# Kernel tuning notes

Measured on AMD Instinct MI355X. Metric: run time of the kernel, lower is better.

## Reference

```python
import jax, jax.numpy as jnp
import numpy as np

N = 50000      # nodes
E = 800000     # edges (before self-loops)
DIN = 128      # input feature dim
DOUT = 128     # per-head output dim
H = 4          # heads (concat=False -> mean over heads)
SLOPE = 0.2    # PyG GATConv default negative_slope


def setup_inputs() -> dict:
    key = jax.random.key(0)
    k1, k2, k3, k4, k5 = jax.random.split(key, 5)
    x = jax.random.normal(k1, (N, DIN), dtype=jnp.float32)
    edge_index = jax.random.randint(k2, (2, E), 0, N)
    W = jax.random.normal(k3, (DIN, H * DOUT), dtype=jnp.float32) / np.sqrt(DIN).astype(np.float32)
    att_src = jax.random.normal(k4, (H, DOUT), dtype=jnp.float32) * 0.1
    att_dst = jax.random.normal(k5, (H, DOUT), dtype=jnp.float32) * 0.1
    return {"x": x, "edge_index": edge_index, "W": W, "att_src": att_src, "att_dst": att_dst}


def _gat(x, W, att_src, att_dst, src, dst):
    h = (x @ W).reshape(N, H, DOUT)                      # [N,H,C] shared lin for src/dst
    a_s = jnp.einsum('nhc,hc->nh', h, att_src)           # [N,H]
    a_d = jnp.einsum('nhc,hc->nh', h, att_dst)           # [N,H]
    logits = jax.nn.leaky_relu(a_s[src] + a_d[dst], SLOPE)   # [Etot,H]
    m = jax.ops.segment_max(logits, dst, num_segments=N)     # segment softmax (stable)
    e = jnp.exp(logits - m[dst])
    denom = jax.ops.segment_sum(e, dst, num_segments=N)
    alpha = e / (denom[dst] + 1e-16)                         # [Etot,H]
    out = jax.ops.segment_sum(alpha[:, :, None] * h[src], dst, num_segments=N)  # [N,H,C]
    return out.mean(axis=1)                                   # concat=False -> average heads


def reference(x, edge_index, W, att_src, att_dst):
    loop = jnp.arange(N, dtype=edge_index.dtype)          # add_self_loops=True (PyG default)
    src = jnp.concatenate([edge_index[0], loop])
    dst = jnp.concatenate([edge_index[1], loop])
    return _gat(x, W, att_src, att_dst, src, dst)
```

## Files before the change

### kernel.cpp

```cpp
#include <hip/hip_runtime.h>

#define NN 50000
#define EE 800000
#define ETOT (EE + NN)
#define MAXD 192
#define NBK 49
#define CAP 20480
#define CH 4096

typedef _Float16 f16x8 __attribute__((ext_vector_type(8)));
typedef _Float16 f16x2 __attribute__((ext_vector_type(2)));
typedef float f32x4 __attribute__((ext_vector_type(4)));
typedef unsigned int u32x4 __attribute__((ext_vector_type(4)));

__device__ __forceinline__ float lrelu(float v) { return v > 0.f ? v : 0.2f * v; }
__device__ __forceinline__ unsigned int pack2(float a, float b) {
  unsigned short lo = __builtin_bit_cast(unsigned short, (_Float16)a);
  unsigned short hi = __builtin_bit_cast(unsigned short, (_Float16)b);
  return (unsigned int)lo | ((unsigned int)hi << 16);
}

__global__ void k_prep(const float* __restrict__ W,
                       const float* __restrict__ att_s,
                       const float* __restrict__ att_d,
                       unsigned short* __restrict__ Bt,
                       float* __restrict__ WaS, float* __restrict__ WaD,
                       int* __restrict__ bcnt) {
  int gid = blockIdx.x * blockDim.x + threadIdx.x;
  if (gid < NBK) bcnt[gid] = 0;
  if (gid < 128 * 512) {
    int col = gid >> 9, k = gid & 511;
    float v = W[(k & 127) * 512 + (k >> 7) * 128 + col];
    _Float16 hv = (_Float16)v;
    Bt[col * 512 + k] = __builtin_bit_cast(unsigned short, hv);
  }
  if (gid < 512) {
    int k = gid >> 2, h = gid & 3;
    const float* wrow = W + k * 512 + h * 128;
    const float* as = att_s + h * 128;
    const float* ad = att_d + h * 128;
    float ss = 0.f, sd = 0.f;
    for (int c = 0; c < 128; ++c) { float w = wrow[c]; ss += w * as[c]; sd += w * ad[c]; }
    WaS[k * 4 + h] = ss;
    WaD[k * 4 + h] = sd;
  }
}

__global__ __launch_bounds__(256) void k_xcast(const float* __restrict__ x,
                                               const float* __restrict__ WaS,
                                               const float* __restrict__ WaD,
                                               unsigned int* __restrict__ xh,
                                               float* __restrict__ a_s,
                                               float* __restrict__ a_d) {
  __shared__ unsigned long long D[128][33];
  __shared__ float4 wsl[128];
  __shared__ float4 wdl[128];
  int t = threadIdx.x;
  int nb = blockIdx.x * 128;
  if (t < 128) wsl[t] = ((const float4*)WaS)[t];
  else wdl[t - 128] = ((const float4*)WaD)[t - 128];

#pragma unroll
  for (int i = 0; i < 16; ++i) {
    int idx = t + i * 256;
    int n = idx >> 5, c4 = idx & 31;
    int gn = nb + n;
    float4 v = make_float4(0.f, 0.f, 0.f, 0.f);
    if (gn < NN) v = ((const float4*)x)[(size_t)gn * 32 + c4];
    unsigned int lo = pack2(v.x, v.y);
    unsigned int hi = pack2(v.z, v.w);
    if (gn < NN) ((uint2*)xh)[(size_t)gn * 32 + c4] = make_uint2(lo, hi);
    D[n][c4] = (unsigned long long)lo | ((unsigned long long)hi << 32);
  }
  __syncthreads();

  int n = t >> 1, half = t & 1;
  float s0 = 0.f, s1 = 0.f, s2 = 0.f, s3 = 0.f;
  float d0 = 0.f, d1 = 0.f, d2 = 0.f, d3 = 0.f;
#pragma unroll
  for (int p = 0; p < 16; ++p) {
    int c4 = 2 * p + half;
    unsigned long long q = D[n][c4];
    f16x2 lo2 = __builtin_bit_cast(f16x2, (unsigned int)q);
    f16x2 hi2 = __builtin_bit_cast(f16x2, (unsigned int)(q >> 32));
    float f0 = (float)lo2[0], f1 = (float)lo2[1];
    float f2 = (float)hi2[0], f3 = (float)hi2[1];
    int c = c4 * 4;
    float4 w0 = wsl[c], w1 = wsl[c + 1], w2 = wsl[c + 2], w3 = wsl[c + 3];
    s0 += f0 * w0.x + f1 * w1.x + f2 * w2.x + f3 * w3.x;
    s1 += f0 * w0.y + f1 * w1.y + f2 * w2.y + f3 * w3.y;
    s2 += f0 * w0.z + f1 * w1.z + f2 * w2.z + f3 * w3.z;
    s3 += f0 * w0.w + f1 * w1.w + f2 * w2.w + f3 * w3.w;
    float4 v0 = wdl[c], v1 = wdl[c + 1], v2 = wdl[c + 2], v3 = wdl[c + 3];
    d0 += f0 * v0.x + f1 * v1.x + f2 * v2.x + f3 * v3.x;
    d1 += f0 * v0.y + f1 * v1.y + f2 * v2.y + f3 * v3.y;
    d2 += f0 * v0.z + f1 * v1.z + f2 * v2.z + f3 * v3.z;
    d3 += f0 * v0.w + f1 * v1.w + f2 * v2.w + f3 * v3.w;
  }
  s0 += __shfl_xor(s0, 1); s1 += __shfl_xor(s1, 1);
  s2 += __shfl_xor(s2, 1); s3 += __shfl_xor(s3, 1);
  d0 += __shfl_xor(d0, 1); d1 += __shfl_xor(d1, 1);
  d2 += __shfl_xor(d2, 1); d3 += __shfl_xor(d3, 1);
  int gn = nb + n;
  if (half == 0 && gn < NN) {
    *(float4*)(a_s + gn * 4) = make_float4(s0, s1, s2, s3);
    *(float4*)(a_d + gn * 4) = make_float4(d0, d1, d2, d3);
  }
}

__global__ __launch_bounds__(256) void k_p1(const int* __restrict__ ei,
                                            int* __restrict__ bcnt,
                                            unsigned int* __restrict__ ebuf) {
  __shared__ int cnt[NBK];
  __shared__ int gbase[NBK];
  int t = threadIdx.x;
  int e0 = blockIdx.x * CH;
  for (int i = t; i < NBK; i += 256) cnt[i] = 0;
  __syncthreads();
#pragma unroll
  for (int i = 0; i < CH / 256; ++i) {
    int e = e0 + t + i * 256;
    if (e < ETOT) {
      int d = (e < EE) ? ei[EE + e] : (e - EE);
      atomicAdd(&cnt[d >> 10], 1);
    }
  }
  __syncthreads();
  for (int i = t; i < NBK; i += 256) {
    gbase[i] = (cnt[i] > 0) ? atomicAdd(&bcnt[i], cnt[i]) : 0;
    cnt[i] = 0;
  }
  __syncthreads();
#pragma unroll
  for (int i = 0; i < CH / 256; ++i) {
    int e = e0 + t + i * 256;
    if (e < ETOT) {
      int s, d;
      if (e < EE) { s = ei[e]; d = ei[EE + e]; } else { s = d = e - EE; }
      int b = d >> 10;
      int idx = gbase[b] + atomicAdd(&cnt[b], 1);
      if (idx < CAP)
        ebuf[b * CAP + idx] = (unsigned int)s | ((unsigned int)(d & 1023) << 16);
    }
  }
}

__global__ __launch_bounds__(256) void k_p2(const unsigned int* __restrict__ ebuf,
                                            const int* __restrict__ bcnt,
                                            int* __restrict__ rs,
                                            unsigned short* __restrict__ perm16) {
  __shared__ int cnt[1024];
  __shared__ int loc[1024];
  __shared__ int sb[256];
  __shared__ unsigned short out16[CAP];
  __shared__ int basesh;
  int b = blockIdx.x, t = threadIdx.x;

  if (t < 64) {
    int v = (t < NBK) ? bcnt[t] : 0;
    int incl = v;
#pragma unroll
    for (int off = 1; off < 64; off <<= 1) {
      int u = __shfl_up(incl, off);
      if ((int)(t) >= off) incl += u;
    }
    if (t == b) basesh = incl - v;
  }
  for (int i = t; i < 1024; i += 256) cnt[i] = 0;
  __syncthreads();

  int base = basesh;
  int m = min(bcnt[b], CAP);
  const unsigned int* rec = ebuf + b * CAP;
  for (int i = t; i < m; i += 256) atomicAdd(&cnt[rec[i] >> 16], 1);
  __syncthreads();

  int i0 = t * 4;
  int c0 = cnt[i0], c1 = cnt[i0 + 1], c2 = cnt[i0 + 2], c3 = cnt[i0 + 3];
  int tt = c0 + c1 + c2 + c3;
  sb[t] = tt;
  __syncthreads();
  for (int off = 1; off < 256; off <<= 1) {
    int v = (t >= off) ? sb[t - off] : 0;
    __syncthreads();
    sb[t] += v;
    __syncthreads();
  }
  int ex = sb[t] - tt;
  loc[i0] = ex;
  loc[i0 + 1] = ex + c0;
  loc[i0 + 2] = ex + c0 + c1;
  loc[i0 + 3] = ex + c0 + c1 + c2;
  int d0 = b * 1024;
#pragma unroll
  for (int k = 0; k < 4; ++k) {
    int gi = d0 + i0 + k;
    if (gi <= NN) {
      int lv;
      if (k == 0) lv = ex;
      else if (k == 1) lv = ex + c0;
      else if (k == 2) lv = ex + c0 + c1;
      else lv = ex + c0 + c1 + c2;
      rs[gi] = base + lv;
    }
  }
  if (b == NBK - 1 && t == 0) rs[NN] = base + m;
  cnt[i0] = 0; cnt[i0 + 1] = 0; cnt[i0 + 2] = 0; cnt[i0 + 3] = 0;
  __syncthreads();

  for (int i = t; i < m; i += 256) {
    unsigned int r = rec[i];
    int dl = r >> 16;
    int rk = atomicAdd(&cnt[dl], 1);
    out16[loc[dl] + rk] = (unsigned short)(r & 0xffffu);
  }
  __syncthreads();
  for (int i = t; i < m; i += 256) perm16[base + i] = out16[i];
}

__global__ __launch_bounds__(256) void k_aggz(const float* __restrict__ a_s,
                                              const float* __restrict__ a_d,
                                              const unsigned int* __restrict__ xh,
                                              const int* __restrict__ rs,
                                              const unsigned short* __restrict__ perm16,
                                              unsigned int* __restrict__ zbuf) {
  __shared__ unsigned short sn_s[4][MAXD];
  __shared__ float4 w_s[4][MAXD];
  int wave = threadIdx.x >> 6, lane = threadIdx.x & 63;
  int n = blockIdx.x * 4 + wave;
  float4 ad = *(const float4*)(a_d + n * 4);
  int s = rs[n], e = rs[n + 1];
  int deg = e - s;
  bool fast = (deg <= MAXD);

  float t0 = 0.f, t1 = 0.f, t2 = 0.f, t3 = 0.f;
  if (fast) {
    for (int j = lane; j < deg; j += 64) {
      int sn = perm16[s + j];
      sn_s[wave][j] = (unsigned short)sn;
      float4 as = *(const float4*)(a_s + sn * 4);
      float e0 = __expf(lrelu(as.x + ad.x));
      float e1 = __expf(lrelu(as.y + ad.y));
      float e2 = __expf(lrelu(as.z + ad.z));
      float e3 = __expf(lrelu(as.w + ad.w));
      w_s[wave][j] = make_float4(e0, e1, e2, e3);
      t0 += e0; t1 += e1; t2 += e2; t3 += e3;
    }
  } else {
    for (int base = s; base < e; base += 64) {
      int j = base + lane;
      if (j < e) {
        int sn = perm16[j];
        float4 as = *(const float4*)(a_s + sn * 4);
        t0 += __expf(lrelu(as.x + ad.x)); t1 += __expf(lrelu(as.y + ad.y));
        t2 += __expf(lrelu(as.z + ad.z)); t3 += __expf(lrelu(as.w + ad.w));
      }
    }
  }
#pragma unroll
  for (int off = 32; off; off >>= 1) {
    t0 += __shfl_xor(t0, off); t1 += __shfl_xor(t1, off);
    t2 += __shfl_xor(t2, off); t3 += __shfl_xor(t3, off);
  }
  float i0 = 0.25f / (t0 + 1e-16f), i1 = 0.25f / (t1 + 1e-16f);
  float i2 = 0.25f / (t2 + 1e-16f), i3 = 0.25f / (t3 + 1e-16f);
  __syncthreads();

  float za[4][2];
#pragma unroll
  for (int h = 0; h < 4; ++h) { za[h][0] = 0.f; za[h][1] = 0.f; }

  if (fast) {
    int j = 0;
    for (; j + 4 <= deg; j += 4) {
      int s0_ = sn_s[wave][j],     s1_ = sn_s[wave][j + 1];
      int s2_ = sn_s[wave][j + 2], s3_ = sn_s[wave][j + 3];
      float4 w0 = w_s[wave][j],     w1 = w_s[wave][j + 1];
      float4 w2 = w_s[wave][j + 2], w3 = w_s[wave][j + 3];
      unsigned int u0 = xh[s0_ * 64 + lane];
      unsigned int u1 = xh[s1_ * 64 + lane];
      unsigned int u2 = xh[s2_ * 64 + lane];
      unsigned int u3 = xh[s3_ * 64 + lane];
      f16x2 p0 = __builtin_bit_cast(f16x2, u0);
      f16x2 p1 = __builtin_bit_cast(f16x2, u1);
      f16x2 p2 = __builtin_bit_cast(f16x2, u2);
      f16x2 p3 = __builtin_bit_cast(f16x2, u3);
      float a0 = (float)p0[0], b0 = (float)p0[1];
      float a1 = (float)p1[0], b1 = (float)p1[1];
      float a2 = (float)p2[0], b2 = (float)p2[1];
      float a3 = (float)p3[0], b3 = (float)p3[1];
      za[0][0] = fmaf(w0.x, a0, za[0][0]); za[0][1] = fmaf(w0.x, b0, za[0][1]);
      za[1][0] = fmaf(w0.y, a0, za[1][0]); za[1][1] = fmaf(w0.y, b0, za[1][1]);
      za[2][0] = fmaf(w0.z, a0, za[2][0]); za[2][1] = fmaf(w0.z, b0, za[2][1]);
      za[3][0] = fmaf(w0.w, a0, za[3][0]); za[3][1] = fmaf(w0.w, b0, za[3][1]);
      za[0][0] = fmaf(w1.x, a1, za[0][0]); za[0][1] = fmaf(w1.x, b1, za[0][1]);
      za[1][0] = fmaf(w1.y, a1, za[1][0]); za[1][1] = fmaf(w1.y, b1, za[1][1]);
      za[2][0] = fmaf(w1.z, a1, za[2][0]); za[2][1] = fmaf(w1.z, b1, za[2][1]);
      za[3][0] = fmaf(w1.w, a1, za[3][0]); za[3][1] = fmaf(w1.w, b1, za[3][1]);
      za[0][0] = fmaf(w2.x, a2, za[0][0]); za[0][1] = fmaf(w2.x, b2, za[0][1]);
      za[1][0] = fmaf(w2.y, a2, za[1][0]); za[1][1] = fmaf(w2.y, b2, za[1][1]);
      za[2][0] = fmaf(w2.z, a2, za[2][0]); za[2][1] = fmaf(w2.z, b2, za[2][1]);
      za[3][0] = fmaf(w2.w, a2, za[3][0]); za[3][1] = fmaf(w2.w, b2, za[3][1]);
      za[0][0] = fmaf(w3.x, a3, za[0][0]); za[0][1] = fmaf(w3.x, b3, za[0][1]);
      za[1][0] = fmaf(w3.y, a3, za[1][0]); za[1][1] = fmaf(w3.y, b3, za[1][1]);
      za[2][0] = fmaf(w3.z, a3, za[2][0]); za[2][1] = fmaf(w3.z, b3, za[2][1]);
      za[3][0] = fmaf(w3.w, a3, za[3][0]); za[3][1] = fmaf(w3.w, b3, za[3][1]);
    }
    for (; j < deg; ++j) {
      int sa = sn_s[wave][j];
      float4 w = w_s[wave][j];
      unsigned int u = xh[sa * 64 + lane];
      f16x2 p = __builtin_bit_cast(f16x2, u);
      float a = (float)p[0], b = (float)p[1];
      za[0][0] = fmaf(w.x, a, za[0][0]); za[0][1] = fmaf(w.x, b, za[0][1]);
      za[1][0] = fmaf(w.y, a, za[1][0]); za[1][1] = fmaf(w.y, b, za[1][1]);
      za[2][0] = fmaf(w.z, a, za[2][0]); za[2][1] = fmaf(w.z, b, za[2][1]);
      za[3][0] = fmaf(w.w, a, za[3][0]); za[3][1] = fmaf(w.w, b, za[3][1]);
    }
  } else {
    for (int j = s; j < e; ++j) {
      int sn = perm16[j];
      float4 as = *(const float4*)(a_s + sn * 4);
      float w0 = __expf(lrelu(as.x + ad.x));
      float w1 = __expf(lrelu(as.y + ad.y));
      float w2 = __expf(lrelu(as.z + ad.z));
      float w3 = __expf(lrelu(as.w + ad.w));
      unsigned int u = xh[sn * 64 + lane];
      f16x2 p = __builtin_bit_cast(f16x2, u);
      float a = (float)p[0], b = (float)p[1];
      za[0][0] = fmaf(w0, a, za[0][0]); za[0][1] = fmaf(w0, b, za[0][1]);
      za[1][0] = fmaf(w1, a, za[1][0]); za[1][1] = fmaf(w1, b, za[1][1]);
      za[2][0] = fmaf(w2, a, za[2][0]); za[2][1] = fmaf(w2, b, za[2][1]);
      za[3][0] = fmaf(w3, a, za[3][0]); za[3][1] = fmaf(w3, b, za[3][1]);
    }
  }

  float sc[4] = {i0, i1, i2, i3};
#pragma unroll
  for (int h = 0; h < 4; ++h) {
    unsigned short lo = __builtin_bit_cast(unsigned short, (_Float16)(za[h][0] * sc[h]));
    unsigned short hi = __builtin_bit_cast(unsigned short, (_Float16)(za[h][1] * sc[h]));
    zbuf[n * 256 + h * 64 + lane] = (unsigned int)lo | ((unsigned int)hi << 16);
  }
}

__global__ __launch_bounds__(256) void k_gemmz(const unsigned short* __restrict__ zbuf,
                                               const unsigned short* __restrict__ Bt,
                                               float* __restrict__ out) {
  __shared__ u32x4 Al[1024];
  __shared__ u32x4 Bl[2048];
  int m0 = blockIdx.x * 64;
  int wave = threadIdx.x >> 6, lane = threadIdx.x & 63;
  int wm = (wave >> 1) * 32, wn = (wave & 1) * 64;
  int lr = lane & 15, lk = lane >> 4;

  f32x4 acc[2][4];
#pragma unroll
  for (int mi = 0; mi < 2; ++mi)
#pragma unroll
    for (int ni = 0; ni < 4; ++ni) acc[mi][ni] = (f32x4){0.f, 0.f, 0.f, 0.f};

  for (int t = 0; t < 4; ++t) {
#pragma unroll
    for (int i = 0; i < 4; ++i) {
      int id = threadIdx.x + 256 * i;
      int row = id >> 4, kc = id & 15;
      int grow = m0 + row;
      u32x4 v = {0u, 0u, 0u, 0u};
      if (grow < NN) v = *(const u32x4*)((const char*)zbuf + grow * 1024 + t * 256 + kc * 16);
      Al[row * 16 + (kc ^ (row & 7))] = v;
    }
#pragma unroll
    for (int i = 0; i < 8; ++i) {
      int id = threadIdx.x + 256 * i;
      int col = id >> 4, kc = id & 15;
      u32x4 v = *(const u32x4*)((const char*)Bt + col * 1024 + t * 256 + kc * 16);
      Bl[col * 16 + (kc ^ (col & 7))] = v;
    }
    __syncthreads();
#pragma unroll
    for (int ks = 0; ks < 4; ++ks) {
      f16x8 af[2], bf[4];
#pragma unroll
      for (int mi = 0; mi < 2; ++mi) {
        int r = wm + mi * 16 + lr;
        af[mi] = __builtin_bit_cast(f16x8, Al[r * 16 + ((ks * 4 + lk) ^ (r & 7))]);
      }
#pragma unroll
      for (int ni = 0; ni < 4; ++ni) {
        int c = wn + ni * 16 + lr;
        bf[ni] = __builtin_bit_cast(f16x8, Bl[c * 16 + ((ks * 4 + lk) ^ (c & 7))]);
      }
#pragma unroll
      for (int mi = 0; mi < 2; ++mi)
#pragma unroll
        for (int ni = 0; ni < 4; ++ni)
          acc[mi][ni] = __builtin_amdgcn_mfma_f32_16x16x32_f16(af[mi], bf[ni], acc[mi][ni], 0, 0, 0);
    }
    __syncthreads();
  }

  int cr = lk * 4;
#pragma unroll
  for (int mi = 0; mi < 2; ++mi) {
#pragma unroll
    for (int j = 0; j < 4; ++j) {
      int row = m0 + wm + mi * 16 + cr + j;
      if (row < NN) {
#pragma unroll
        for (int ni = 0; ni < 4; ++ni) {
          int col = wn + ni * 16 + lr;
          out[row * 128 + col] = acc[mi][ni][j];
        }
      }
    }
  }
}

extern "C" void kernel_launch(void* const* d_in, const int* in_sizes, int n_in,
                              void* d_out, int out_size, void* d_ws, size_t ws_size,
                              hipStream_t stream) {
  const float* x = (const float*)d_in[0];
  const int* ei = (const int*)d_in[1];
  const float* W = (const float*)d_in[2];
  const float* att_s = (const float*)d_in[3];
  const float* att_d = (const float*)d_in[4];
  float* out = (float*)d_out;
  char* ws = (char*)d_ws;

  unsigned int* xh = (unsigned int*)(ws + 0);
  unsigned int* zbuf = (unsigned int*)(ws + 12800000);
  unsigned int* ebuf = (unsigned int*)(ws + 12800000);
  unsigned short* Bt = (unsigned short*)(ws + 64000000);
  float* WaS = (float*)(ws + 64131072);
  float* WaD = (float*)(ws + 64133120);
  float* a_s = (float*)(ws + 64135168);
  float* a_d = (float*)(ws + 64935168);
  int* rs = (int*)(ws + 65735168);
  int* bcnt = (int*)(ws + 65935360);
  unsigned short* perm16 = (unsigned short*)(ws + 65935616);

  k_prep<<<256, 256, 0, stream>>>(W, att_s, att_d, Bt, WaS, WaD, bcnt);
  k_xcast<<<(NN + 127) / 128, 256, 0, stream>>>(x, WaS, WaD, xh, a_s, a_d);
  k_p1<<<(ETOT + CH - 1) / CH, 256, 0, stream>>>(ei, bcnt, ebuf);
  k_p2<<<NBK, 256, 0, stream>>>(ebuf, bcnt, rs, perm16);
  k_aggz<<<NN / 4, 256, 0, stream>>>(a_s, a_d, xh, rs, perm16, zbuf);
  k_gemmz<<<(NN + 63) / 64, 256, 0, stream>>>((const unsigned short*)zbuf, Bt, out);
}
```

Measured before the change: 142.9 us.

## Fuse aggregation with GEMM and merge cast with edge bucketing

Aggregation now writes the per-head weighted fp16 sums for 32 nodes into shared memory, and an MFMA GEMM reads them from there in the same kernel. This removes the global zbuf round trip and one launch. The x cast/attention-score kernel is merged with the first edge-bucketing pass, and the buckets shrink from 1024 to 256 destinations, giving 196 bucket blocks in the second pass for more parallelism. The fused kernel reads B directly from global memory without LDS staging, and MAXD is lowered to 96, so more high-degree nodes take the slow path.

```diff
diff --git a/kernel.cpp b/kernel.cpp
--- a/kernel.cpp
+++ b/kernel.cpp
@@ -3,14 +3,16 @@
 #define NN 50000
 #define EE 800000
 #define ETOT (EE + NN)
-#define MAXD 192
-#define NBK 49
-#define CAP 20480
-#define CH 4096
+#define MAXD 96
+#define NBK 196
+#define CAP 6144
+#define CHX 2304
+#define TM 32
 
 typedef _Float16 f16x8 __attribute__((ext_vector_type(8)));
 typedef _Float16 f16x2 __attribute__((ext_vector_type(2)));
 typedef float f32x4 __attribute__((ext_vector_type(4)));
+typedef float f32x2 __attribute__((ext_vector_type(2)));
 typedef unsigned int u32x4 __attribute__((ext_vector_type(4)));
 
 __device__ __forceinline__ float lrelu(float v) { return v > 0.f ? v : 0.2f * v; }
@@ -46,19 +48,25 @@
   }
 }
 
-__global__ __launch_bounds__(256) void k_xcast(const float* __restrict__ x,
-                                               const float* __restrict__ WaS,
-                                               const float* __restrict__ WaD,
-                                               unsigned int* __restrict__ xh,
-                                               float* __restrict__ a_s,
-                                               float* __restrict__ a_d) {
+__global__ __launch_bounds__(256) void k_xcast_p1(const float* __restrict__ x,
+                                                  const float* __restrict__ WaS,
+                                                  const float* __restrict__ WaD,
+                                                  const int* __restrict__ ei,
+                                                  unsigned int* __restrict__ xh,
+                                                  float* __restrict__ a_s,
+                                                  float* __restrict__ a_d,
+                                                  int* __restrict__ bcnt,
+                                                  unsigned int* __restrict__ ebuf) {
   __shared__ unsigned long long D[128][33];
   __shared__ float4 wsl[128];
   __shared__ float4 wdl[128];
+  __shared__ int cnt[NBK];
+  __shared__ int gbase[NBK];
   int t = threadIdx.x;
   int nb = blockIdx.x * 128;
   if (t < 128) wsl[t] = ((const float4*)WaS)[t];
   else wdl[t - 128] = ((const float4*)WaD)[t - 128];
+  for (int i = t; i < NBK; i += 256) cnt[i] = 0;
 
 #pragma unroll
   for (int i = 0; i < 16; ++i) {
@@ -74,55 +82,48 @@
   }
   __syncthreads();
 
-  int n = t >> 1, half = t & 1;
-  float s0 = 0.f, s1 = 0.f, s2 = 0.f, s3 = 0.f;
-  float d0 = 0.f, d1 = 0.f, d2 = 0.f, d3 = 0.f;
-#pragma unroll
-  for (int p = 0; p < 16; ++p) {
-    int c4 = 2 * p + half;
-    unsigned long long q = D[n][c4];
-    f16x2 lo2 = __builtin_bit_cast(f16x2, (unsigned int)q);
-    f16x2 hi2 = __builtin_bit_cast(f16x2, (unsigned int)(q >> 32));
-    float f0 = (float)lo2[0], f1 = (float)lo2[1];
-    float f2 = (float)hi2[0], f3 = (float)hi2[1];
-    int c = c4 * 4;
-    float4 w0 = wsl[c], w1 = wsl[c + 1], w2 = wsl[c + 2], w3 = wsl[c + 3];
-    s0 += f0 * w0.x + f1 * w1.x + f2 * w2.x + f3 * w3.x;
-    s1 += f0 * w0.y + f1 * w1.y + f2 * w2.y + f3 * w3.y;
-    s2 += f0 * w0.z + f1 * w1.z + f2 * w2.z + f3 * w3.z;
-    s3 += f0 * w0.w + f1 * w1.w + f2 * w2.w + f3 * w3.w;
-    float4 v0 = wdl[c], v1 = wdl[c + 1], v2 = wdl[c + 2], v3 = wdl[c + 3];
-    d0 += f0 * v0.x + f1 * v1.x + f2 * v2.x + f3 * v3.x;
-    d1 += f0 * v0.y + f1 * v1.y + f2 * v2.y + f3 * v3.y;
-    d2 += f0 * v0.z + f1 * v1.z + f2 * v2.z + f3 * v3.z;
-    d3 += f0 * v0.w + f1 * v1.w + f2 * v2.w + f3 * v3.w;
-  }
-  s0 += __shfl_xor(s0, 1); s1 += __shfl_xor(s1, 1);
-  s2 += __shfl_xor(s2, 1); s3 += __shfl_xor(s3, 1);
-  d0 += __shfl_xor(d0, 1); d1 += __shfl_xor(d1, 1);
-  d2 += __shfl_xor(d2, 1); d3 += __shfl_xor(d3, 1);
-  int gn = nb + n;
-  if (half == 0 && gn < NN) {
-    *(float4*)(a_s + gn * 4) = make_float4(s0, s1, s2, s3);
-    *(float4*)(a_d + gn * 4) = make_float4(d0, d1, d2, d3);
-  }
-}
-
-__global__ __launch_bounds__(256) void k_p1(const int* __restrict__ ei,
-                                            int* __restrict__ bcnt,
-                                            unsigned int* __restrict__ ebuf) {
-  __shared__ int cnt[NBK];
-  __shared__ int gbase[NBK];
-  int t = threadIdx.x;
-  int e0 = blockIdx.x * CH;
-  for (int i = t; i < NBK; i += 256) cnt[i] = 0;
-  __syncthreads();
-#pragma unroll
-  for (int i = 0; i < CH / 256; ++i) {
-    int e = e0 + t + i * 256;
+  {
+    int n = t >> 1, half = t & 1;
+    float s0 = 0.f, s1 = 0.f, s2 = 0.f, s3 = 0.f;
+    float d0 = 0.f, d1 = 0.f, d2 = 0.f, d3 = 0.f;
+#pragma unroll
+    for (int p = 0; p < 16; ++p) {
+      int c4 = 2 * p + half;
+      unsigned long long q = D[n][c4];
+      f16x2 lo2 = __builtin_bit_cast(f16x2, (unsigned int)q);
+      f16x2 hi2 = __builtin_bit_cast(f16x2, (unsigned int)(q >> 32));
+      float f0 = (float)lo2[0], f1 = (float)lo2[1];
+      float f2 = (float)hi2[0], f3 = (float)hi2[1];
+      int c = c4 * 4;
+      float4 w0 = wsl[c], w1 = wsl[c + 1], w2 = wsl[c + 2], w3 = wsl[c + 3];
+      s0 += f0 * w0.x + f1 * w1.x + f2 * w2.x + f3 * w3.x;
+      s1 += f0 * w0.y + f1 * w1.y + f2 * w2.y + f3 * w3.y;
+      s2 += f0 * w0.z + f1 * w1.z + f2 * w2.z + f3 * w3.z;
+      s3 += f0 * w0.w + f1 * w1.w + f2 * w2.w + f3 * w3.w;
+      float4 v0 = wdl[c], v1 = wdl[c + 1], v2 = wdl[c + 2], v3 = wdl[c + 3];
+      d0 += f0 * v0.x + f1 * v1.x + f2 * v2.x + f3 * v3.x;
+      d1 += f0 * v0.y + f1 * v1.y + f2 * v2.y + f3 * v3.y;
+      d2 += f0 * v0.z + f1 * v1.z + f2 * v2.z + f3 * v3.z;
+      d3 += f0 * v0.w + f1 * v1.w + f2 * v2.w + f3 * v3.w;
+    }
+    s0 += __shfl_xor(s0, 1); s1 += __shfl_xor(s1, 1);
+    s2 += __shfl_xor(s2, 1); s3 += __shfl_xor(s3, 1);
+    d0 += __shfl_xor(d0, 1); d1 += __shfl_xor(d1, 1);
+    d2 += __shfl_xor(d2, 1); d3 += __shfl_xor(d3, 1);
+    int gn = nb + n;
+    if (half == 0 && gn < NN) {
+      *(float4*)(a_s + gn * 4) = make_float4(s0, s1, s2, s3);
+      *(float4*)(a_d + gn * 4) = make_float4(d0, d1, d2, d3);
+    }
+  }
+
+  int e0 = blockIdx.x * CHX;
+#pragma unroll
+  for (int k = 0; k < CHX / 256; ++k) {
+    int e = e0 + t + k * 256;
     if (e < ETOT) {
       int d = (e < EE) ? ei[EE + e] : (e - EE);
-      atomicAdd(&cnt[d >> 10], 1);
+      atomicAdd(&cnt[d >> 8], 1);
     }
   }
   __syncthreads();
@@ -132,15 +133,15 @@
   }
   __syncthreads();
 #pragma unroll
-  for (int i = 0; i < CH / 256; ++i) {
-    int e = e0 + t + i * 256;
+  for (int k = 0; k < CHX / 256; ++k) {
+    int e = e0 + t + k * 256;
     if (e < ETOT) {
       int s, d;
       if (e < EE) { s = ei[e]; d = ei[EE + e]; } else { s = d = e - EE; }
-      int b = d >> 10;
+      int b = d >> 8;
       int idx = gbase[b] + atomicAdd(&cnt[b], 1);
       if (idx < CAP)
-        ebuf[b * CAP + idx] = (unsigned int)s | ((unsigned int)(d & 1023) << 16);
+        ebuf[(size_t)b * CAP + idx] = (unsigned int)s | ((unsigned int)(d & 255) << 16);
     }
   }
 }
@@ -149,63 +150,48 @@
                                             const int* __restrict__ bcnt,
                                             int* __restrict__ rs,
                                             unsigned short* __restrict__ perm16) {
-  __shared__ int cnt[1024];
-  __shared__ int loc[1024];
   __shared__ int sb[256];
+  __shared__ int loc[256];
+  __shared__ int cnt[256];
   __shared__ unsigned short out16[CAP];
   __shared__ int basesh;
   int b = blockIdx.x, t = threadIdx.x;
 
-  if (t < 64) {
-    int v = (t < NBK) ? bcnt[t] : 0;
-    int incl = v;
-#pragma unroll
-    for (int off = 1; off < 64; off <<= 1) {
-      int u = __shfl_up(incl, off);
-      if ((int)(t) >= off) incl += u;
-    }
-    if (t == b) basesh = incl - v;
-  }
-  for (int i = t; i < 1024; i += 256) cnt[i] = 0;
+  int v = (t < NBK) ? bcnt[t] : 0;
+  sb[t] = v;
+  __syncthreads();
+  for (int off = 1; off < 256; off <<= 1) {
+    int u = (t >= off) ? sb[t - off] : 0;
+    __syncthreads();
+    sb[t] += u;
+    __syncthreads();
+  }
+  if (t == b) basesh = sb[t] - v;
+  cnt[t] = 0;
   __syncthreads();
 
   int base = basesh;
   int m = min(bcnt[b], CAP);
-  const unsigned int* rec = ebuf + b * CAP;
+  int d0 = b * 256;
+  const unsigned int* rec = ebuf + (size_t)b * CAP;
   for (int i = t; i < m; i += 256) atomicAdd(&cnt[rec[i] >> 16], 1);
   __syncthreads();
 
-  int i0 = t * 4;
-  int c0 = cnt[i0], c1 = cnt[i0 + 1], c2 = cnt[i0 + 2], c3 = cnt[i0 + 3];
-  int tt = c0 + c1 + c2 + c3;
-  sb[t] = tt;
+  int c = cnt[t];
+  sb[t] = c;
   __syncthreads();
   for (int off = 1; off < 256; off <<= 1) {
-    int v = (t >= off) ? sb[t - off] : 0;
-    __syncthreads();
-    sb[t] += v;
-    __syncthreads();
-  }
-  int ex = sb[t] - tt;
-  loc[i0] = ex;
-  loc[i0 + 1] = ex + c0;
-  loc[i0 + 2] = ex + c0 + c1;
-  loc[i0 + 3] = ex + c0 + c1 + c2;
-  int d0 = b * 1024;
-#pragma unroll
-  for (int k = 0; k < 4; ++k) {
-    int gi = d0 + i0 + k;
-    if (gi <= NN) {
-      int lv;
-      if (k == 0) lv = ex;
-      else if (k == 1) lv = ex + c0;
-      else if (k == 2) lv = ex + c0 + c1;
-      else lv = ex + c0 + c1 + c2;
-      rs[gi] = base + lv;
-    }
-  }
+    int u = (t >= off) ? sb[t - off] : 0;
+    __syncthreads();
+    sb[t] += u;
+    __syncthreads();
+  }
+  int ex = sb[t] - c;
+  loc[t] = ex;
+  int gi = d0 + t;
+  if (gi < NN) rs[gi] = base + ex;
   if (b == NBK - 1 && t == 0) rs[NN] = base + m;
-  cnt[i0] = 0; cnt[i0 + 1] = 0; cnt[i0 + 2] = 0; cnt[i0 + 3] = 0;
+  cnt[t] = 0;
   __syncthreads();
 
   for (int i = t; i < m; i += 256) {
@@ -218,199 +204,165 @@
   for (int i = t; i < m; i += 256) perm16[base + i] = out16[i];
 }
 
-__global__ __launch_bounds__(256) void k_aggz(const float* __restrict__ a_s,
-                                              const float* __restrict__ a_d,
-                                              const unsigned int* __restrict__ xh,
-                                              const int* __restrict__ rs,
-                                              const unsigned short* __restrict__ perm16,
-                                              unsigned int* __restrict__ zbuf) {
+__global__ __launch_bounds__(256) void k_fused(const float* __restrict__ a_s,
+                                               const float* __restrict__ a_d,
+                                               const unsigned int* __restrict__ xh,
+                                               const int* __restrict__ rs,
+                                               const unsigned short* __restrict__ perm16,
+                                               const unsigned short* __restrict__ Bt,
+                                               float* __restrict__ out) {
+  __shared__ u32x4 Zl[TM * 64];
+  __shared__ float4 w_s[4][MAXD];
   __shared__ unsigned short sn_s[4][MAXD];
-  __shared__ float4 w_s[4][MAXD];
+  unsigned int* Zw = (unsigned int*)Zl;
   int wave = threadIdx.x >> 6, lane = threadIdx.x & 63;
-  int n = blockIdx.x * 4 + wave;
-  float4 ad = *(const float4*)(a_d + n * 4);
-  int s = rs[n], e = rs[n + 1];
-  int deg = e - s;
-  bool fast = (deg <= MAXD);
-
-  float t0 = 0.f, t1 = 0.f, t2 = 0.f, t3 = 0.f;
-  if (fast) {
-    for (int j = lane; j < deg; j += 64) {
-      int sn = perm16[s + j];
-      sn_s[wave][j] = (unsigned short)sn;
-      float4 as = *(const float4*)(a_s + sn * 4);
-      float e0 = __expf(lrelu(as.x + ad.x));
-      float e1 = __expf(lrelu(as.y + ad.y));
-      float e2 = __expf(lrelu(as.z + ad.z));
-      float e3 = __expf(lrelu(as.w + ad.w));
-      w_s[wave][j] = make_float4(e0, e1, e2, e3);
-      t0 += e0; t1 += e1; t2 += e2; t3 += e3;
-    }
-  } else {
-    for (int base = s; base < e; base += 64) {
-      int j = base + lane;
-      if (j < e) {
-        int sn = perm16[j];
+  int m0 = blockIdx.x * TM;
+
+#pragma unroll 1
+  for (int i = 0; i < 8; ++i) {
+    int r = wave * 8 + i;
+    int n = m0 + r;
+    bool valid = (n < NN);
+    int s = 0, deg = 0;
+    float4 ad = make_float4(0.f, 0.f, 0.f, 0.f);
+    if (valid) {
+      s = rs[n];
+      deg = rs[n + 1] - s;
+      ad = *(const float4*)(a_d + n * 4);
+    }
+    bool fast = (deg <= MAXD);
+    float t0 = 0.f, t1 = 0.f, t2 = 0.f, t3 = 0.f;
+    if (fast) {
+      for (int j = lane; j < deg; j += 64) {
+        int sn = perm16[s + j];
+        sn_s[wave][j] = (unsigned short)sn;
+        float4 as = *(const float4*)(a_s + sn * 4);
+        float e0 = __expf(lrelu(as.x + ad.x));
+        float e1 = __expf(lrelu(as.y + ad.y));
+        float e2 = __expf(lrelu(as.z + ad.z));
+        float e3 = __expf(lrelu(as.w + ad.w));
+        w_s[wave][j] = make_float4(e0, e1, e2, e3);
+        t0 += e0; t1 += e1; t2 += e2; t3 += e3;
+      }
+    } else {
+      for (int j = lane; j < deg; j += 64) {
+        int sn = perm16[s + j];
         float4 as = *(const float4*)(a_s + sn * 4);
         t0 += __expf(lrelu(as.x + ad.x)); t1 += __expf(lrelu(as.y + ad.y));
         t2 += __expf(lrelu(as.z + ad.z)); t3 += __expf(lrelu(as.w + ad.w));
       }
     }
-  }
-#pragma unroll
-  for (int off = 32; off; off >>= 1) {
-    t0 += __shfl_xor(t0, off); t1 += __shfl_xor(t1, off);
-    t2 += __shfl_xor(t2, off); t3 += __shfl_xor(t3, off);
-  }
-  float i0 = 0.25f / (t0 + 1e-16f), i1 = 0.25f / (t1 + 1e-16f);
-  float i2 = 0.25f / (t2 + 1e-16f), i3 = 0.25f / (t3 + 1e-16f);
-  __syncthreads();
-
-  float za[4][2];
-#pragma unroll
-  for (int h = 0; h < 4; ++h) { za[h][0] = 0.f; za[h][1] = 0.f; }
-
-  if (fast) {
-    int j = 0;
-    for (; j + 4 <= deg; j += 4) {
-      int s0_ = sn_s[wave][j],     s1_ = sn_s[wave][j + 1];
-      int s2_ = sn_s[wave][j + 2], s3_ = sn_s[wave][j + 3];
-      float4 w0 = w_s[wave][j],     w1 = w_s[wave][j + 1];
-      float4 w2 = w_s[wave][j + 2], w3 = w_s[wave][j + 3];
-      unsigned int u0 = xh[s0_ * 64 + lane];
-      unsigned int u1 = xh[s1_ * 64 + lane];
-      unsigned int u2 = xh[s2_ * 64 + lane];
-      unsigned int u3 = xh[s3_ * 64 + lane];
-      f16x2 p0 = __builtin_bit_cast(f16x2, u0);
-      f16x2 p1 = __builtin_bit_cast(f16x2, u1);
-      f16x2 p2 = __builtin_bit_cast(f16x2, u2);
-      f16x2 p3 = __builtin_bit_cast(f16x2, u3);
-      float a0 = (float)p0[0], b0 = (float)p0[1];
-      float a1 = (float)p1[0], b1 = (float)p1[1];
-      float a2 = (float)p2[0], b2 = (float)p2[1];
-      float a3 = (float)p3[0], b3 = (float)p3[1];
-      za[0][0] = fmaf(w0.x, a0, za[0][0]); za[0][1] = fmaf(w0.x, b0, za[0][1]);
-      za[1][0] = fmaf(w0.y, a0, za[1][0]); za[1][1] = fmaf(w0.y, b0, za[1][1]);
-      za[2][0] = fmaf(w0.z, a0, za[2][0]); za[2][1] = fmaf(w0.z, b0, za[2][1]);
-      za[3][0] = fmaf(w0.w, a0, za[3][0]); za[3][1] = fmaf(w0.w, b0, za[3][1]);
-      za[0][0] = fmaf(w1.x, a1, za[0][0]); za[0][1] = fmaf(w1.x, b1, za[0][1]);
-      za[1][0] = fmaf(w1.y, a1, za[1][0]); za[1][1] = fmaf(w1.y, b1, za[1][1]);
-      za[2][0] = fmaf(w1.z, a1, za[2][0]); za[2][1] = fmaf(w1.z, b1, za[2][1]);
-      za[3][0] = fmaf(w1.w, a1, za[3][0]); za[3][1] = fmaf(w1.w, b1, za[3][1]);
-      za[0][0] = fmaf(w2.x, a2, za[0][0]); za[0][1] = fmaf(w2.x, b2, za[0][1]);
-      za[1][0] = fmaf(w2.y, a2, za[1][0]); za[1][1] = fmaf(w2.y, b2, za[1][1]);
-      za[2][0] = fmaf(w2.z, a2, za[2][0]); za[2][1] = fmaf(w2.z, b2, za[2][1]);
-      za[3][0] = fmaf(w2.w, a2, za[3][0]); za[3][1] = fmaf(w2.w, b2, za[3][1]);
-      za[0][0] = fmaf(w3.x, a3, za[0][0]); za[0][1] = fmaf(w3.x, b3, za[0][1]);
-      za[1][0] = fmaf(w3.y, a3, za[1][0]); za[1][1] = fmaf(w3.y, b3, za[1][1]);
-      za[2][0] = fmaf(w3.z, a3, za[2][0]); za[2][1] = fmaf(w3.z, b3, za[2][1]);
-      za[3][0] = fmaf(w3.w, a3, za[3][0]); za[3][1] = fmaf(w3.w, b3, za[3][1]);
-    }
-    for (; j < deg; ++j) {
-      int sa = sn_s[wave][j];
-      float4 w = w_s[wave][j];
-      unsigned int u = xh[sa * 64 + lane];
-      f16x2 p = __builtin_bit_cast(f16x2, u);
-      float a = (float)p[0], b = (float)p[1];
-      za[0][0] = fmaf(w.x, a, za[0][0]); za[0][1] = fmaf(w.x, b, za[0][1]);
-      za[1][0] = fmaf(w.y, a, za[1][0]); za[1][1] = fmaf(w.y, b, za[1][1]);
-      za[2][0] = fmaf(w.z, a, za[2][0]); za[2][1] = fmaf(w.z, b, za[2][1]);
-      za[3][0] = fmaf(w.w, a, za[3][0]); za[3][1] = fmaf(w.w, b, za[3][1]);
-    }
-  } else {
-    for (int j = s; j < e; ++j) {
-      int sn = perm16[j];
-      float4 as = *(const float4*)(a_s + sn * 4);
-      float w0 = __expf(lrelu(as.x + ad.x));
-      float w1 = __expf(lrelu(as.y + ad.y));
-      float w2 = __expf(lrelu(as.z + ad.z));
-      float w3 = __expf(lrelu(as.w + ad.w));
-      unsigned int u = xh[sn * 64 + lane];
-      f16x2 p = __builtin_bit_cast(f16x2, u);
-      float a = (float)p[0], b = (float)p[1];
-      za[0][0] = fmaf(w0, a, za[0][0]); za[0][1] = fmaf(w0, b, za[0][1]);
-      za[1][0] = fmaf(w1, a, za[1][0]); za[1][1] = fmaf(w1, b, za[1][1]);
-      za[2][0] = fmaf(w2, a, za[2][0]); za[2][1] = fmaf(w2, b, za[2][1]);
-      za[3][0] = fmaf(w3, a, za[3][0]); za[3][1] = fmaf(w3, b, za[3][1]);
-    }
-  }
-
-  float sc[4] = {i0, i1, i2, i3};
-#pragma unroll
-  for (int h = 0; h < 4; ++h) {
-    unsigned short lo = __builtin_bit_cast(unsigned short, (_Float16)(za[h][0] * sc[h]));
-    unsigned short hi = __builtin_bit_cast(unsigned short, (_Float16)(za[h][1] * sc[h]));
-    zbuf[n * 256 + h * 64 + lane] = (unsigned int)lo | ((unsigned int)hi << 16);
-  }
-}
-
-__global__ __launch_bounds__(256) void k_gemmz(const unsigned short* __restrict__ zbuf,
-                                               const unsigned short* __restrict__ Bt,
-                                               float* __restrict__ out) {
-  __shared__ u32x4 Al[1024];
-  __shared__ u32x4 Bl[2048];
-  int m0 = blockIdx.x * 64;
-  int wave = threadIdx.x >> 6, lane = threadIdx.x & 63;
-  int wm = (wave >> 1) * 32, wn = (wave & 1) * 64;
+#pragma unroll
+    for (int off = 32; off; off >>= 1) {
+      t0 += __shfl_xor(t0, off); t1 += __shfl_xor(t1, off);
+      t2 += __shfl_xor(t2, off); t3 += __shfl_xor(t3, off);
+    }
+    float sc0 = 0.25f / (t0 + 1e-16f), sc1 = 0.25f / (t1 + 1e-16f);
+    float sc2 = 0.25f / (t2 + 1e-16f), sc3 = 0.25f / (t3 + 1e-16f);
+    __syncthreads();
+
+    f32x2 za0 = {0.f, 0.f}, za1 = {0.f, 0.f}, za2 = {0.f, 0.f}, za3 = {0.f, 0.f};
+    if (fast) {
+      int j = 0;
+      for (; j + 4 <= deg; j += 4) {
+        int s0_ = sn_s[wave][j],     s1_ = sn_s[wave][j + 1];
+        int s2_ = sn_s[wave][j + 2], s3_ = sn_s[wave][j + 3];
+        float4 w0 = w_s[wave][j],     w1 = w_s[wave][j + 1];
+        float4 w2 = w_s[wave][j + 2], w3 = w_s[wave][j + 3];
+        unsigned int u0 = xh[s0_ * 64 + lane];
+        unsigned int u1 = xh[s1_ * 64 + lane];
+        unsigned int u2 = xh[s2_ * 64 + lane];
+        unsigned int u3 = xh[s3_ * 64 + lane];
+        f16x2 p0 = __builtin_bit_cast(f16x2, u0);
+        f16x2 p1 = __builtin_bit_cast(f16x2, u1);
+        f16x2 p2 = __builtin_bit_cast(f16x2, u2);
+        f16x2 p3 = __builtin_bit_cast(f16x2, u3);
+        f32x2 x0 = {(float)p0[0], (float)p0[1]};
+        f32x2 x1 = {(float)p1[0], (float)p1[1]};
+        f32x2 x2 = {(float)p2[0], (float)p2[1]};
+        f32x2 x3 = {(float)p3[0], (float)p3[1]};
+        za0 += w0.x * x0; za1 += w0.y * x0; za2 += w0.z * x0; za3 += w0.w * x0;
+        za0 += w1.x * x1; za1 += w1.y * x1; za2 += w1.z * x1; za3 += w1.w * x1;
+        za0 += w2.x * x2; za1 += w2.y * x2; za2 += w2.z * x2; za3 += w2.w * x2;
+        za0 += w3.x * x3; za1 += w3.y * x3; za2 += w3.z * x3; za3 += w3.w * x3;
+      }
+      for (; j < deg; ++j) {
+        int sa = sn_s[wave][j];
+        float4 w = w_s[wave][j];
+        unsigned int u = xh[sa * 64 + lane];
+        f16x2 p = __builtin_bit_cast(f16x2, u);
+        f32x2 xv = {(float)p[0], (float)p[1]};
+        za0 += w.x * xv; za1 += w.y * xv; za2 += w.z * xv; za3 += w.w * xv;
+      }
+    } else {
+      for (int j = 0; j < deg; ++j) {
+        int sn = perm16[s + j];
+        float4 as = *(const float4*)(a_s + sn * 4);
+        float w0 = __expf(lrelu(as.x + ad.x));
+        float w1 = __expf(lrelu(as.y + ad.y));
+        float w2 = __expf(lrelu(as.z + ad.z));
+        float w3 = __expf(lrelu(as.w + ad.w));
+        unsigned int u = xh[sn * 64 + lane];
+        f16x2 p = __builtin_bit_cast(f16x2, u);
+        f32x2 xv = {(float)p[0], (float)p[1]};
+        za0 += w0 * xv; za1 += w1 * xv; za2 += w2 * xv; za3 += w3 * xv;
+      }
+    }
+
+    unsigned int pk0 = pack2(za0[0] * sc0, za0[1] * sc0);
+    unsigned int pk1 = pack2(za1[0] * sc1, za1[1] * sc1);
+    unsigned int pk2 = pack2(za2[0] * sc2, za2[1] * sc2);
+    unsigned int pk3 = pack2(za3[0] * sc3, za3[1] * sc3);
+    if (!valid) { pk0 = 0u; pk1 = 0u; pk2 = 0u; pk3 = 0u; }
+    int rb = r & 7;
+    int ct = lane >> 2, sub = lane & 3;
+    Zw[r * 256 + (((0 * 16 + ct) ^ rb) << 2) + sub] = pk0;
+    Zw[r * 256 + (((1 * 16 + ct) ^ rb) << 2) + sub] = pk1;
+    Zw[r * 256 + (((2 * 16 + ct) ^ rb) << 2) + sub] = pk2;
+    Zw[r * 256 + (((3 * 16 + ct) ^ rb) << 2) + sub] = pk3;
+  }
+  __syncthreads();
+
   int lr = lane & 15, lk = lane >> 4;
-
-  f32x4 acc[2][4];
+  int n0w = wave * 32;
+  const u32x4* Bv = (const u32x4*)Bt;
+  f32x4 acc[2][2];
 #pragma unroll
   for (int mi = 0; mi < 2; ++mi)
 #pragma unroll
-    for (int ni = 0; ni < 4; ++ni) acc[mi][ni] = (f32x4){0.f, 0.f, 0.f, 0.f};
-
-  for (int t = 0; t < 4; ++t) {
-#pragma unroll
-    for (int i = 0; i < 4; ++i) {
-      int id = threadIdx.x + 256 * i;
-      int row = id >> 4, kc = id & 15;
-      int grow = m0 + row;
-      u32x4 v = {0u, 0u, 0u, 0u};
-      if (grow < NN) v = *(const u32x4*)((const char*)zbuf + grow * 1024 + t * 256 + kc * 16);
-      Al[row * 16 + (kc ^ (row & 7))] = v;
-    }
-#pragma unroll
-    for (int i = 0; i < 8; ++i) {
-      int id = threadIdx.x + 256 * i;
-      int col = id >> 4, kc = id & 15;
-      u32x4 v = *(const u32x4*)((const char*)Bt + col * 1024 + t * 256 + kc * 16);
-      Bl[col * 16 + (kc ^ (col & 7))] = v;
-    }
-    __syncthreads();
-#pragma unroll
-    for (int ks = 0; ks < 4; ++ks) {
-      f16x8 af[2], bf[4];
-#pragma unroll
-      for (int mi = 0; mi < 2; ++mi) {
-        int r = wm + mi * 16 + lr;
-        af[mi] = __builtin_bit_cast(f16x8, Al[r * 16 + ((ks * 4 + lk) ^ (r & 7))]);
-      }
-#pragma unroll
-      for (int ni = 0; ni < 4; ++ni) {
-        int c = wn + ni * 16 + lr;
-        bf[ni] = __builtin_bit_cast(f16x8, Bl[c * 16 + ((ks * 4 + lk) ^ (c & 7))]);
-      }
-#pragma unroll
-      for (int mi = 0; mi < 2; ++mi)
-#pragma unroll
-        for (int ni = 0; ni < 4; ++ni)
-          acc[mi][ni] = __builtin_amdgcn_mfma_f32_16x16x32_f16(af[mi], bf[ni], acc[mi][ni], 0, 0, 0);
-    }
-    __syncthreads();
+    for (int ni = 0; ni < 2; ++ni) acc[mi][ni] = (f32x4){0.f, 0.f, 0.f, 0.f};
+
+#pragma unroll
+  for (int kk = 0; kk < 16; ++kk) {
+    f16x8 af[2], bf[2];
+#pragma unroll
+    for (int mi = 0; mi < 2; ++mi) {
+      int r2 = mi * 16 + lr;
+      af[mi] = __builtin_bit_cast(f16x8, Zl[r2 * 64 + ((kk * 4 + lk) ^ (r2 & 7))]);
+    }
+#pragma unroll
+    for (int ni = 0; ni < 2; ++ni) {
+      int cix = n0w + ni * 16 + lr;
+      bf[ni] = __builtin_bit_cast(f16x8, Bv[cix * 64 + kk * 4 + lk]);
+    }
+#pragma unroll
+    for (int mi = 0; mi < 2; ++mi)
+#pragma unroll
+      for (int ni = 0; ni < 2; ++ni)
+        acc[mi][ni] = __builtin_amdgcn_mfma_f32_16x16x32_f16(af[mi], bf[ni], acc[mi][ni], 0, 0, 0);
   }
 
   int cr = lk * 4;
 #pragma unroll
   for (int mi = 0; mi < 2; ++mi) {
 #pragma unroll
-    for (int j = 0; j < 4; ++j) {
-      int row = m0 + wm + mi * 16 + cr + j;
+    for (int j2 = 0; j2 < 4; ++j2) {
+      int row = m0 + mi * 16 + cr + j2;
       if (row < NN) {
 #pragma unroll
-        for (int ni = 0; ni < 4; ++ni) {
-          int col = wn + ni * 16 + lr;
-          out[row * 128 + col] = acc[mi][ni][j];
+        for (int ni = 0; ni < 2; ++ni) {
+          int col = n0w + ni * 16 + lr;
+          out[row * 128 + col] = acc[mi][ni][j2];
         }
       }
     }
@@ -429,21 +381,18 @@
   char* ws = (char*)d_ws;
 
   unsigned int* xh = (unsigned int*)(ws + 0);
-  unsigned int* zbuf = (unsigned int*)(ws + 12800000);
   unsigned int* ebuf = (unsigned int*)(ws + 12800000);
-  unsigned short* Bt = (unsigned short*)(ws + 64000000);
-  float* WaS = (float*)(ws + 64131072);
-  float* WaD = (float*)(ws + 64133120);
-  float* a_s = (float*)(ws + 64135168);
-  float* a_d = (float*)(ws + 64935168);
-  int* rs = (int*)(ws + 65735168);
-  int* bcnt = (int*)(ws + 65935360);
-  unsigned short* perm16 = (unsigned short*)(ws + 65935616);
+  unsigned short* Bt = (unsigned short*)(ws + 17616896);
+  float* WaS = (float*)(ws + 17747968);
+  float* WaD = (float*)(ws + 17750016);
+  float* a_s = (float*)(ws + 17752064);
+  float* a_d = (float*)(ws + 18552064);
+  int* rs = (int*)(ws + 19352064);
+  int* bcnt = (int*)(ws + 19552256);
+  unsigned short* perm16 = (unsigned short*)(ws + 19553280);
 
   k_prep<<<256, 256, 0, stream>>>(W, att_s, att_d, Bt, WaS, WaD, bcnt);
-  k_xcast<<<(NN + 127) / 128, 256, 0, stream>>>(x, WaS, WaD, xh, a_s, a_d);
-  k_p1<<<(ETOT + CH - 1) / CH, 256, 0, stream>>>(ei, bcnt, ebuf);
+  k_xcast_p1<<<(NN + 127) / 128, 256, 0, stream>>>(x, WaS, WaD, ei, xh, a_s, a_d, bcnt, ebuf);
   k_p2<<<NBK, 256, 0, stream>>>(ebuf, bcnt, rs, perm16);
-  k_aggz<<<NN / 4, 256, 0, stream>>>(a_s, a_d, xh, rs, perm16, zbuf);
-  k_gemmz<<<(NN + 63) / 64, 256, 0, stream>>>((const unsigned short*)zbuf, Bt, out);
-}
+  k_fused<<<(NN + TM - 1) / TM, 256, 0, stream>>>(a_s, a_d, xh, rs, perm16, Bt, out);
+}
```

Result: slower. 156.4 us (+9.4%).
